# Kernel optimization log

Measured on AMD Instinct MI355X. Metric: run time of the kernel, lower is better.

Reference implementation:

```python
import jax, jax.numpy as jnp
import numpy as np
import math

B, S, L, D, H, NL, FF, MAXP = 4, 200, 256, 256, 8, 2, 1024, 512
VOC, EDIM, BERT_D, LBL = 50000, 50, 768, 20
DH = D // H
NEG = -1e15


def _pe_table():
    # get_embedding(max_seq_len, hidden, rel_pos_init=0): sinusoidal over 0..2*MAXP
    half = D // 2
    freq = jnp.exp(jnp.arange(half, dtype=jnp.float32) * (-math.log(10000.0) / (half - 1)))
    pos = jnp.arange(2 * MAXP + 1, dtype=jnp.float32)[:, None] * freq[None, :]
    return jnp.concatenate([jnp.sin(pos), jnp.cos(pos)], axis=1)  # [2*MAXP+1, D]


def _ln(x, g, b, eps=1e-5):
    m = x.mean(-1, keepdims=True)
    v = jnp.mean((x - m) ** 2, -1, keepdims=True)
    return (x - m) * jax.lax.rsqrt(v + eps) * g + b


def _forward(lattice, bigrams, seq_len, lex_num, pos_s, pos_e,
             bert_embed, lat_table, big_table, Wc, bc, Wl, bl, W_fus, b_fus,
             Wq, bq, Wk, bk, Wv, bv, Wr, br, u, vb, Wo, bo,
             ln1_g, ln1_b, W1, b1, W2, b2, ln2_g, ln2_b, Wout, bout):
    raw = lat_table[lattice]                                        # [B,L,EDIM]
    big = jnp.pad(big_table[bigrams], ((0, 0), (0, L - S), (0, 0)))  # pad to lattice len
    bert = jnp.pad(bert_embed, ((0, 0), (0, L - S), (0, 0)))
    raw_char = jnp.concatenate([raw, big, bert], -1)                # [B,L,868]
    idx = jnp.arange(L)
    char_mask = idx[None, :] < seq_len[:, None]
    tot_mask = idx[None, :] < (seq_len + lex_num)[:, None]
    lex_mask = tot_mask & (~char_mask)
    # embed_char masked to char positions, embed_lex masked to lexicon positions
    x = (raw_char @ Wc + bc) * char_mask[..., None] + (raw @ Wl + bl) * lex_mask[..., None]

    # four-way relative position fusion ('ff'): relu(Linear(cat[pe_ss,pe_se,pe_es,pe_ee]))
    # computed as sum of four gathered pre-projected tables (same math, no 4D concat)
    pe = _pe_table()
    T = jnp.einsum('pe,keo->kpo', pe, W_fus.reshape(4, D, D))       # [4, 2*MAXP+1, D]
    ss = pos_s[:, :, None] - pos_s[:, None, :] + MAXP
    se = pos_s[:, :, None] - pos_e[:, None, :] + MAXP
    es = pos_e[:, :, None] - pos_s[:, None, :] + MAXP
    ee = pos_e[:, :, None] - pos_e[:, None, :] + MAXP
    rel = jax.nn.relu(T[0][ss] + T[1][se] + T[2][es] + T[3][ee] + b_fus)  # [B,L,L,D]

    scale = 1.0 / math.sqrt(DH)
    for l in range(NL):
        qh = (x @ Wq[l] + bq[l]).reshape(B, L, H, DH).transpose(0, 2, 1, 3)
        kh = (x @ Wk[l] + bk[l]).reshape(B, L, H, DH).transpose(0, 2, 1, 3)
        vh = (x @ Wv[l] + bv[l]).reshape(B, L, H, DH).transpose(0, 2, 1, 3)
        rh = (rel @ Wr[l] + br[l]).reshape(B, L, L, H, DH)
        # Transformer-XL style: A+C with content bias u, B+D with position bias v
        AC = jnp.einsum('bhqd,bhkd->bhqk', qh + u[l][None, :, None, :], kh)
        BD = jnp.einsum('bhqd,bqkhd->bhqk', qh + vb[l][None, :, None, :], rh)
        score = (AC + BD) * scale
        score = jnp.where(tot_mask[:, None, None, :], score, NEG)
        attn = jax.nn.softmax(score, -1)
        out = jnp.einsum('bhqk,bhkd->bhqd', attn, vh).transpose(0, 2, 1, 3).reshape(B, L, D)
        x = _ln(out @ Wo[l] + bo[l] + x, ln1_g[l], ln1_b[l])
        h = jax.nn.relu(x @ W1[l] + b1[l]) @ W2[l] + b2[l]
        x = _ln(h + x, ln2_g[l], ln2_b[l])
    return x[:, :S] @ Wout + bout                                   # emission logits [B,S,LBL]


def setup_inputs() -> dict:
    key = jax.random.key(0)
    ks = jax.random.split(key, 32)
    p = lambda i, sh, s=0.02: jax.random.normal(ks[i], sh, jnp.float32) * s
    inp = {}
    inp['lattice'] = jax.random.randint(ks[0], (B, L), 1, VOC)
    inp['bigrams'] = jax.random.randint(ks[1], (B, S), 1, VOC)
    inp['seq_len'] = jax.random.randint(ks[2], (B,), 150, S + 1)
    inp['lex_num'] = jax.random.randint(ks[3], (B,), 20, L - S + 1)
    s_lex = jax.random.randint(ks[4], (B, L - S), 0, 180)
    e_lex = s_lex + jax.random.randint(ks[5], (B, L - S), 1, 20)
    ar = jnp.broadcast_to(jnp.arange(S), (B, S))
    inp['pos_s'] = jnp.concatenate([ar, s_lex], 1)
    inp['pos_e'] = jnp.concatenate([ar, e_lex], 1)
    inp['target'] = jax.random.randint(ks[6], (B, S), 0, LBL)
    inp['bert_embed'] = p(7, (B, S, BERT_D), 1.0)
    inp['lat_table'] = p(8, (VOC, EDIM), 1.0)
    inp['big_table'] = p(9, (VOC, EDIM), 1.0)
    cin = 2 * EDIM + BERT_D
    inp['Wc'] = p(10, (cin, D)); inp['bc'] = jnp.zeros((D,))
    inp['Wl'] = p(11, (EDIM, D)); inp['bl'] = jnp.zeros((D,))
    inp['W_fus'] = p(12, (4 * D, D)); inp['b_fus'] = jnp.zeros((D,))
    inp['Wq'] = p(13, (NL, D, D)); inp['bq'] = jnp.zeros((NL, D))
    inp['Wk'] = p(14, (NL, D, D)); inp['bk'] = jnp.zeros((NL, D))
    inp['Wv'] = p(15, (NL, D, D)); inp['bv'] = jnp.zeros((NL, D))
    inp['Wr'] = p(16, (NL, D, D)); inp['br'] = jnp.zeros((NL, D))
    inp['u'] = p(17, (NL, H, DH)); inp['vb'] = p(18, (NL, H, DH))
    inp['Wo'] = p(19, (NL, D, D)); inp['bo'] = jnp.zeros((NL, D))
    inp['ln1_g'] = jnp.ones((NL, D)); inp['ln1_b'] = jnp.zeros((NL, D))
    inp['W1'] = p(20, (NL, D, FF)); inp['b1'] = jnp.zeros((NL, FF))
    inp['W2'] = p(21, (NL, FF, D)); inp['b2'] = jnp.zeros((NL, D))
    inp['ln2_g'] = jnp.ones((NL, D)); inp['ln2_b'] = jnp.zeros((NL, D))
    inp['Wout'] = p(22, (D, LBL)); inp['bout'] = jnp.zeros((LBL,))
    return inp


def reference(lattice, bigrams, seq_len, lex_num, pos_s, pos_e, target,
              bert_embed, lat_table, big_table, Wc, bc, Wl, bl, W_fus, b_fus,
              Wq, bq, Wk, bk, Wv, bv, Wr, br, u, vb, Wo, bo,
              ln1_g, ln1_b, W1, b1, W2, b2, ln2_g, ln2_b, Wout, bout):
    # target is consumed by the downstream CRF loss (omitted); emission logits returned
    return _forward(lattice, bigrams, seq_len, lex_num, pos_s, pos_e,
                    bert_embed, lat_table, big_table, Wc, bc, Wl, bl, W_fus, b_fus,
                    Wq, bq, Wk, bk, Wv, bv, Wr, br, u, vb, Wo, bo,
                    ln1_g, ln1_b, W1, b1, W2, b2, ln2_g, ln2_b, Wout, bout)
```

## Files before the change

kernel.cpp:

```cpp
#include <hip/hip_runtime.h>
#include <math.h>

#define NB 4
#define SS 200
#define LT 256
#define DD 256
#define NH 8
#define NLAYER 2
#define FFD 1024
#define BERTD 768
#define NEGINF -1e15f
#define SCL 0.17677669529663687f

typedef __attribute__((ext_vector_type(8))) short bf16x8;
typedef __attribute__((ext_vector_type(4))) float f32x4;
typedef __attribute__((ext_vector_type(8))) unsigned short u16x8;

__device__ inline float bf2f(unsigned short h) {
    union { unsigned int u; float f; } v; v.u = ((unsigned int)h) << 16; return v.f;
}
__device__ inline unsigned short f2bf(float x) {
    union { float f; unsigned int u; } v; v.f = x;
    unsigned int r = v.u + 0x7fffu + ((v.u >> 16) & 1u);
    return (unsigned short)(r >> 16);
}
__device__ inline void split2(float x, unsigned short& h, unsigned short& l) {
    h = f2bf(x); l = f2bf(x - bf2f(h));
}

__global__ void gather_v3(const int* __restrict__ lattice, const int* __restrict__ bigrams,
                          const int* __restrict__ seq_len, const int* __restrict__ lex_num,
                          const float* __restrict__ bert, const float* __restrict__ lat_t,
                          const float* __restrict__ big_t,
                          unsigned short* __restrict__ Gh, unsigned short* __restrict__ Gl)
{
    const int row = blockIdx.x, t = threadIdx.x;
    const int b = row >> 8, l = row & 255;
    const int sl = seq_len[b], tl = sl + lex_num[b];
    const float mC = (l < sl) ? 1.f : 0.f;
    const float mL = (l >= sl && l < tl) ? 1.f : 0.f;
    const int lat = lattice[row];
    const int big = (l < SS) ? bigrams[b*SS + l] : 0;
    for (int i = t; i < 1024; i += 256) {
        float v;
        if (i < 50)        v = lat_t[lat*50 + i] * mC;
        else if (i < 100)  v = (l < SS) ? big_t[big*50 + (i-50)] * mC : 0.f;
        else if (i < 868)  v = (l < SS) ? bert[(b*SS + l)*BERTD + (i-100)] * mC : 0.f;
        else if (i < 918)  v = lat_t[lat*50 + (i-868)] * mL;
        else if (i == 918) v = mC;
        else if (i == 919) v = mL;
        else               v = 0.f;
        unsigned short hh, ll; split2(v, hh, ll);
        Gh[(size_t)row*1024 + i] = hh; Gl[(size_t)row*1024 + i] = ll;
    }
}

__global__ void wcomb_kernel(const float* __restrict__ Wc, const float* __restrict__ bc,
                             const float* __restrict__ Wl, const float* __restrict__ bl,
                             float* __restrict__ Wcomb)
{
    const int r = blockIdx.x, t = threadIdx.x;
    float v;
    if (r < 868)       v = Wc[r*DD + t];
    else if (r < 918)  v = Wl[(r-868)*DD + t];
    else if (r == 918) v = bc[t];
    else if (r == 919) v = bl[t];
    else               v = 0.f;
    Wcomb[r*DD + t] = v;
}

__global__ void pe_v3(unsigned short* __restrict__ PEh, unsigned short* __restrict__ PEl)
{
    const int p = blockIdx.x, t = threadIdx.x;
    float v = 0.f;
    if (p <= 1024) {
        const float fr = expf(-(float)(t & 127) * (9.210340371976184f / 127.0f));
        const float arg = (float)p * fr;
        v = (t < 128) ? sinf(arg) : cosf(arg);
    }
    unsigned short hh, ll; split2(v, hh, ll);
    PEh[p*DD + t] = hh; PEl[p*DD + t] = ll;
}

__global__ void smallpack(const float* __restrict__ bq, const float* __restrict__ bk,
                          const float* __restrict__ bv, const float* __restrict__ b_fus,
                          float* __restrict__ bqkv, float* __restrict__ bfus4)
{
    const int t = threadIdx.x;
    for (int l = 0; l < NLAYER; ++l) {
        bqkv[l*768 + t]       = bq[l*DD + t];
        bqkv[l*768 + 256 + t] = bk[l*DD + t];
        bqkv[l*768 + 512 + t] = bv[l*DD + t];
    }
    bfus4[t] = b_fus[t];
    bfus4[256 + t] = 0.f; bfus4[512 + t] = 0.f; bfus4[768 + t] = 0.f;
}

__global__ void vrbias_kernel(const float* __restrict__ vb, const float* __restrict__ Wr,
                              float* __restrict__ bias_vr)
{
    const int lh = blockIdx.x, t = threadIdx.x;
    const int l = lh >> 3, h = lh & 7;
    float acc = 0.f;
    #pragma unroll 8
    for (int d = 0; d < 32; ++d)
        acc += vb[l*DD + h*32 + d] * Wr[(size_t)l*DD*DD + (h*32 + d)*DD + t];
    bias_vr[lh*DD + t] = acc;
}

__global__ void trans_all(const float* __restrict__ Wcomb, const float* __restrict__ Wq,
                          const float* __restrict__ Wk, const float* __restrict__ Wv,
                          const float* __restrict__ Wo, const float* __restrict__ W1,
                          const float* __restrict__ W2, const float* __restrict__ Wfus,
                          const float* __restrict__ Wr,
                          unsigned short* WcombT_h, unsigned short* WcombT_l,
                          unsigned short* WqkvT_h,  unsigned short* WqkvT_l,
                          unsigned short* WoT_h,    unsigned short* WoT_l,
                          unsigned short* W1T_h,    unsigned short* W1T_l,
                          unsigned short* W2T_h,    unsigned short* W2T_l,
                          unsigned short* WfusT_h,  unsigned short* WfusT_l,
                          unsigned short* WrB_h,    unsigned short* WrB_l)
{
    const int z = blockIdx.z, y = blockIdx.y, tx = blockIdx.x, t = threadIdx.x;
    const float* src; unsigned short *dh, *dl; int K, N;
    switch (z) {
        case 0: if (y) return; K = 1024; N = 256; src = Wcomb; dh = WcombT_h; dl = WcombT_l; break;
        case 1: { if (y >= 6) return; int l = y/3, s = y%3; K = 256; N = 256;
                  src = (s==0 ? Wq : s==1 ? Wk : Wv) + l*65536;
                  dh = WqkvT_h + (l*768 + s*256)*256; dl = WqkvT_l + (l*768 + s*256)*256; } break;
        case 2: if (y >= 2) return; K = 256; N = 256;  src = Wo + y*65536;  dh = WoT_h + y*65536;  dl = WoT_l + y*65536;  break;
        case 3: if (y >= 2) return; K = 256; N = 1024; src = W1 + y*262144; dh = W1T_h + y*262144; dl = W1T_l + y*262144; break;
        case 4: if (y >= 2) return; K = 1024; N = 256; src = W2 + y*262144; dh = W2T_h + y*262144; dl = W2T_l + y*262144; break;
        case 5: if (y >= 4) return; K = 256; N = 256;  src = Wfus + y*65536; dh = WfusT_h + y*65536; dl = WfusT_l + y*65536; break;
        case 6: { if (y >= 16) return; int l = y >> 3, h = y & 7; K = 32; N = 256;
                  src = Wr + (size_t)l*65536 + h*32*256;
                  dh = WrB_h + y*8192; dl = WrB_l + y*8192; } break;
        default: return;
    }
    const int tiles_x = N >> 5;
    const int tn = tx % tiles_x, tk = tx / tiles_x;
    if (tk >= (K >> 5)) return;
    __shared__ float s[32][33];
    const int lr = t >> 5, lc = t & 31;
    #pragma unroll
    for (int i = 0; i < 4; ++i)
        s[lr + 8*i][lc] = src[(size_t)(tk*32 + lr + 8*i)*N + tn*32 + lc];
    __syncthreads();
    #pragma unroll
    for (int i = 0; i < 4; ++i) {
        const int n = tn*32 + lr + 8*i, k = tk*32 + lc;
        unsigned short hh, ll; split2(s[lc][lr + 8*i], hh, ll);
        dh[(size_t)n*K + k] = hh;
        dl[(size_t)n*K + k] = ll;
    }
}

template<int BK, bool RELU, bool EMIT>
__global__ __launch_bounds__(256) void gemm_v3(
    const unsigned short* __restrict__ Ah, const unsigned short* __restrict__ Al,
    const unsigned short* __restrict__ Bh, const unsigned short* __restrict__ Bl,
    const float* __restrict__ bias, const float* __restrict__ resid,
    float* __restrict__ C, unsigned short* __restrict__ Ch, unsigned short* __restrict__ Cl,
    int M, int N, int K, int lda, int ldc, int aZ, int bZ, int cZ, int biasZ)
{
    constexpr int LDK = BK + 8;
    __shared__ unsigned short AhS[64*LDK], AlS[64*LDK];
    __shared__ unsigned short BhS[64*LDK], BlS[64*LDK];
    const int z = blockIdx.z;
    Ah += (size_t)z * aZ; Al += (size_t)z * aZ;
    Bh += (size_t)z * bZ; Bl += (size_t)z * bZ;
    C  += (size_t)z * cZ;
    if (EMIT) { Ch += (size_t)z * cZ; Cl += (size_t)z * cZ; }
    if (bias) bias += (size_t)z * biasZ;

    const int t = threadIdx.x;
    const int row0 = blockIdx.y * 64, col0 = blockIdx.x * 64;
    const int lane = t & 63, w = t >> 6;
    const int wm = w >> 1, wn = w & 1;
    const int fr = lane & 15, fq = lane >> 4;
    const int sr = t >> 2, sc0 = (t & 3) * (BK/4);

    f32x4 acc[2][2];
    #pragma unroll
    for (int i = 0; i < 2; ++i)
        #pragma unroll
        for (int j = 0; j < 2; ++j) acc[i][j] = (f32x4){0.f, 0.f, 0.f, 0.f};

    for (int k0 = 0; k0 < K; k0 += BK) {
        #pragma unroll
        for (int i = 0; i < BK/32; ++i) {
            const int c = sc0 + i*8;
            *(u16x8*)&AhS[sr*LDK + c] = *(const u16x8*)&Ah[(size_t)(row0+sr)*lda + k0 + c];
            *(u16x8*)&AlS[sr*LDK + c] = *(const u16x8*)&Al[(size_t)(row0+sr)*lda + k0 + c];
            *(u16x8*)&BhS[sr*LDK + c] = *(const u16x8*)&Bh[(size_t)(col0+sr)*K + k0 + c];
            *(u16x8*)&BlS[sr*LDK + c] = *(const u16x8*)&Bl[(size_t)(col0+sr)*K + k0 + c];
        }
        __syncthreads();
        #pragma unroll
        for (int ks = 0; ks < BK/32; ++ks) {
            const int ko = ks*32 + fq*8;
            const bf16x8 ah0 = *(const bf16x8*)&AhS[(wm*32 + fr)*LDK + ko];
            const bf16x8 ah1 = *(const bf16x8*)&AhS[(wm*32 + 16 + fr)*LDK + ko];
            const bf16x8 al0 = *(const bf16x8*)&AlS[(wm*32 + fr)*LDK + ko];
            const bf16x8 al1 = *(const bf16x8*)&AlS[(wm*32 + 16 + fr)*LDK + ko];
            #pragma unroll
            for (int nt = 0; nt < 2; ++nt) {
                const int nb = (wn*32 + nt*16 + fr)*LDK + ko;
                const bf16x8 bh = *(const bf16x8*)&BhS[nb];
                const bf16x8 bl = *(const bf16x8*)&BlS[nb];
                acc[0][nt] = __builtin_amdgcn_mfma_f32_16x16x32_bf16(ah0, bh, acc[0][nt], 0, 0, 0);
                acc[0][nt] = __builtin_amdgcn_mfma_f32_16x16x32_bf16(ah0, bl, acc[0][nt], 0, 0, 0);
                acc[0][nt] = __builtin_amdgcn_mfma_f32_16x16x32_bf16(al0, bh, acc[0][nt], 0, 0, 0);
                acc[1][nt] = __builtin_amdgcn_mfma_f32_16x16x32_bf16(ah1, bh, acc[1][nt], 0, 0, 0);
                acc[1][nt] = __builtin_amdgcn_mfma_f32_16x16x32_bf16(ah1, bl, acc[1][nt], 0, 0, 0);
                acc[1][nt] = __builtin_amdgcn_mfma_f32_16x16x32_bf16(al1, bh, acc[1][nt], 0, 0, 0);
            }
        }
        __syncthreads();
    }
    #pragma unroll
    for (int mt = 0; mt < 2; ++mt) {
        #pragma unroll
        for (int nt = 0; nt < 2; ++nt) {
            const int gcol = col0 + wn*32 + nt*16 + fr;
            const float bv = bias ? bias[gcol] : 0.f;
            #pragma unroll
            for (int r = 0; r < 4; ++r) {
                const int grow = row0 + wm*32 + mt*16 + fq*4 + r;
                float v = acc[mt][nt][r] + bv;
                if (resid) v += resid[(size_t)grow*ldc + gcol];
                if (RELU)  v = fmaxf(v, 0.f);
                C[(size_t)grow*ldc + gcol] = v;
                if (EMIT) {
                    unsigned short hh, ll; split2(v, hh, ll);
                    Ch[(size_t)grow*ldc + gcol] = hh;
                    Cl[(size_t)grow*ldc + gcol] = ll;
                }
            }
        }
    }
}

__global__ void rcc_split(const float* __restrict__ Tn,
                          unsigned short* __restrict__ Rh, unsigned short* __restrict__ Rl)
{
    const int p = blockIdx.x, t = threadIdx.x;
    const float v = Tn[(size_t)p*1024 + t] + Tn[(size_t)p*1024 + 256 + t]
                  + Tn[(size_t)p*1024 + 512 + t] + Tn[(size_t)p*1024 + 768 + t];
    unsigned short hh, ll; split2(fmaxf(v, 0.f), hh, ll);
    Rh[p*DD + t] = hh; Rl[p*DD + t] = ll;
}

__global__ __launch_bounds__(256) void attn_v4(
    const float* __restrict__ qkvb, const float* __restrict__ qr,
    const float* __restrict__ Tn, const float* __restrict__ Dcc,
    const int* __restrict__ pos_s, const int* __restrict__ pos_e,
    const int* __restrict__ seq_len, const int* __restrict__ lex_num,
    const float* __restrict__ u, float* __restrict__ ob,
    unsigned short* __restrict__ obh, unsigned short* __restrict__ obl)
{
    __shared__ float qu[256];
    __shared__ float qrl[NH][260];
    __shared__ float sc[NH][264];
    __shared__ float acb[NH][264];
    __shared__ float relb[32][260];
    __shared__ float red[2048];
    float* DccL = &relb[0][0];

    const int t = threadIdx.x, row = blockIdx.x;
    const int b = row >> 8, q = row & 255;
    const int totlen = seq_len[b] + lex_num[b];
    if (q >= SS && q >= totlen) {
        ob[row*DD + t] = 0.f; obh[row*DD + t] = 0; obl[row*DD + t] = 0;
        return;
    }
    const bool qc = (q < SS);
    const int gstart = qc ? SS : 0;

    qu[t] = qkvb[(size_t)row*768 + t] + u[t];
    if (totlen > gstart) {
        #pragma unroll
        for (int h = 0; h < NH; ++h) qrl[h][t] = qr[(size_t)row*2048 + h*256 + t];
    }
    if (qc && t < SS) {
        #pragma unroll
        for (int h = 0; h < NH; ++h)
            DccL[h*SS + t] = Dcc[((size_t)h*1024 + row)*448 + q + t];
    }
    const int ps_q = pos_s[row], pe_q = pos_e[row];
    const int* psb = pos_s + b*LT;
    const int* peb = pos_e + b*LT;
    __syncthreads();

    {
        const int h = t & 7, k0 = t >> 3;
        const float4* qp = (const float4*)&qu[h*32];
        #pragma unroll
        for (int pass = 0; pass < 8; ++pass) {
            const int kg = pass*32 + k0;
            if (kg < totlen) {
                const float4* kp = (const float4*)&qkvb[(size_t)(b*LT + kg)*768 + 256 + h*32];
                float ac = 0.f;
                #pragma unroll
                for (int d4 = 0; d4 < 8; ++d4) {
                    const float4 kv = kp[d4], qv = qp[d4];
                    ac += kv.x*qv.x + kv.y*qv.y + kv.z*qv.z + kv.w*qv.w;
                }
                if (qc && kg < SS) sc[h][kg] = (ac + DccL[h*SS + (SS-1) - kg]) * SCL;
                else               acb[h][kg] = ac;
            } else {
                sc[h][kg] = NEGINF;
            }
        }
    }
    __syncthreads();

    const int gs0 = gstart & ~31;
    for (int K0 = gs0; K0 < totlen; K0 += 32) {
        {
            const int r = t >> 3, c4 = (t & 7)*4;
            const int kg = K0 + r;
            if (kg >= gstart && kg < totlen) {
                const int sk = psb[kg], ek = peb[kg];
                const float* t0 = Tn + (size_t)(ps_q - sk + 512)*1024;
                const float* t1 = Tn + (size_t)(ps_q - ek + 512)*1024 + 256;
                const float* t2 = Tn + (size_t)(pe_q - sk + 512)*1024 + 512;
                const float* t3 = Tn + (size_t)(pe_q - ek + 512)*1024 + 768;
                #pragma unroll
                for (int i = 0; i < 8; ++i) {
                    const int e = i*32 + c4;
                    const float4 a = *(const float4*)&t0[e];
                    const float4 bb = *(const float4*)&t1[e];
                    const float4 c = *(const float4*)&t2[e];
                    const float4 d = *(const float4*)&t3[e];
                    float4 v;
                    v.x = fmaxf(a.x + bb.x + c.x + d.x, 0.f);
                    v.y = fmaxf(a.y + bb.y + c.y + d.y, 0.f);
                    v.z = fmaxf(a.z + bb.z + c.z + d.z, 0.f);
                    v.w = fmaxf(a.w + bb.w + c.w + d.w, 0.f);
                    *(float4*)&relb[r][e] = v;
                }
            }
        }
        __syncthreads();
        {
            const int dk = t & 31, seg = t >> 5;
            const int kg = K0 + dk;
            if (kg >= gstart && kg < totlen) {
                float a[8] = {0.f,0.f,0.f,0.f,0.f,0.f,0.f,0.f};
                const int e0 = seg*32;
                #pragma unroll
                for (int e4 = 0; e4 < 8; ++e4) {
                    const float4 r4 = *(const float4*)&relb[dk][e0 + e4*4];
                    #pragma unroll
                    for (int h = 0; h < 8; ++h) {
                        const float4 q4 = *(const float4*)&qrl[h][e0 + e4*4];
                        a[h] += r4.x*q4.x + r4.y*q4.y + r4.z*q4.z + r4.w*q4.w;
                    }
                }
                float4* rb = (float4*)&red[(seg*32 + dk)*8];
                rb[0] = make_float4(a[0], a[1], a[2], a[3]);
                rb[1] = make_float4(a[4], a[5], a[6], a[7]);
            }
        }
        __syncthreads();
        {
            const int k = t >> 3, h = t & 7;
            const int kg = K0 + k;
            if (kg >= gstart && kg < totlen) {
                float s = 0.f;
                #pragma unroll
                for (int g = 0; g < 8; ++g) s += red[g*256 + t];
                sc[h][kg] = (s + acb[h][kg]) * SCL;
            }
        }
        __syncthreads();
    }

    {
        const int g = t >> 5, ln = t & 31;
        float vals[8];
        float m = -INFINITY;
        #pragma unroll
        for (int i = 0; i < 8; ++i) {
            const int kidx = ln + 32*i;
            vals[i] = (kidx < totlen) ? sc[g][kidx] : NEGINF;
            m = fmaxf(m, vals[i]);
        }
        #pragma unroll
        for (int off = 16; off >= 1; off >>= 1) m = fmaxf(m, __shfl_xor(m, off, 32));
        float sum = 0.f;
        #pragma unroll
        for (int i = 0; i < 8; ++i) { vals[i] = expf(vals[i] - m); sum += vals[i]; }
        #pragma unroll
        for (int off = 16; off >= 1; off >>= 1) sum += __shfl_xor(sum, off, 32);
        const float inv = 1.0f / sum;
        #pragma unroll
        for (int i = 0; i < 8; ++i) sc[g][ln + 32*i] = vals[i] * inv;
    }
    __syncthreads();
    {
        const int j4 = (t & 63)*4, kr = t >> 6;
        const int h = j4 >> 5;
        float4 acc = make_float4(0.f, 0.f, 0.f, 0.f);
        const float* vp = qkvb + (size_t)(b*LT)*768 + 512 + j4;
        for (int k = kr; k < totlen; k += 4) {
            const float p = sc[h][k];
            const float4 v = *(const float4*)&vp[(size_t)k*768];
            acc.x += p*v.x; acc.y += p*v.y; acc.z += p*v.z; acc.w += p*v.w;
        }
        *(float4*)&red[kr*256 + j4] = acc;
    }
    __syncthreads();
    {
        const float v = red[t] + red[256 + t] + red[512 + t] + red[768 + t];
        ob[row*DD + t] = v;
        unsigned short hh, ll; split2(v, hh, ll);
        obh[row*DD + t] = hh; obl[row*DD + t] = ll;
    }
}

template<bool EMIT>
__global__ void ln_v3(const float* __restrict__ in, const float* __restrict__ g,
                      const float* __restrict__ bb, float* __restrict__ out,
                      unsigned short* __restrict__ oh, unsigned short* __restrict__ ol)
{
    __shared__ float red[4];
    const int t = threadIdx.x, row = blockIdx.x;
    const float v = in[row*DD + t];
    float s = v;
    #pragma unroll
    for (int off = 32; off >= 1; off >>= 1) s += __shfl_xor(s, off, 64);
    if ((t & 63) == 0) red[t >> 6] = s;
    __syncthreads();
    const float m = (red[0] + red[1] + red[2] + red[3]) * (1.0f/256.0f);
    __syncthreads();
    const float d = v - m;
    float s2 = d*d;
    #pragma unroll
    for (int off = 32; off >= 1; off >>= 1) s2 += __shfl_xor(s2, off, 64);
    if ((t & 63) == 0) red[t >> 6] = s2;
    __syncthreads();
    const float var = (red[0] + red[1] + red[2] + red[3]) * (1.0f/256.0f);
    const float o = d * rsqrtf(var + 1e-5f) * g[t] + bb[t];
    out[row*DD + t] = o;
    if (EMIT) {
        unsigned short hh, ll; split2(o, hh, ll);
        oh[row*DD + t] = hh; ol[row*DD + t] = ll;
    }
}

__global__ void out_kernel(const float* __restrict__ x, const float* __restrict__ Wout,
                           const float* __restrict__ bout, float* __restrict__ out)
{
    __shared__ float xs[256];
    const int t = threadIdx.x, row = blockIdx.x;
    const int b = row / SS, s = row % SS;
    const float* xr = x + (b*LT + s)*DD;
    for (int i = t; i < DD; i += 64) xs[i] = xr[i];
    __syncthreads();
    if (t < 20) {
        float acc = bout[t];
        for (int d = 0; d < DD; ++d) acc += xs[d] * Wout[d*20 + t];
        out[row*20 + t] = acc;
    }
}

extern "C" void kernel_launch(void* const* d_in, const int* in_sizes, int n_in,
                              void* d_out, int out_size, void* d_ws, size_t ws_size,
                              hipStream_t stream)
{
    const int*   lattice = (const int*)d_in[0];
    const int*   bigrams = (const int*)d_in[1];
    const int*   seq_len = (const int*)d_in[2];
    const int*   lex_num = (const int*)d_in[3];
    const int*   pos_s   = (const int*)d_in[4];
    const int*   pos_e   = (const int*)d_in[5];
    const float* bert    = (const float*)d_in[7];
    const float* lat_t   = (const float*)d_in[8];
    const float* big_t   = (const float*)d_in[9];
    const float* Wc      = (const float*)d_in[10];
    const float* bc      = (const float*)d_in[11];
    const float* Wl      = (const float*)d_in[12];
    const float* bl      = (const float*)d_in[13];
    const float* W_fus   = (const float*)d_in[14];
    const float* b_fus   = (const float*)d_in[15];
    const float* Wq      = (const float*)d_in[16];
    const float* bq      = (const float*)d_in[17];
    const float* Wk      = (const float*)d_in[18];
    const float* bk      = (const float*)d_in[19];
    const float* Wv      = (const float*)d_in[20];
    const float* bv      = (const float*)d_in[21];
    const float* Wr      = (const float*)d_in[22];
    const float* u_bias  = (const float*)d_in[24];
    const float* v_bias  = (const float*)d_in[25];
    const float* Wo      = (const float*)d_in[26];
    const float* bo      = (const float*)d_in[27];
    const float* ln1g    = (const float*)d_in[28];
    const float* ln1b    = (const float*)d_in[29];
    const float* W1      = (const float*)d_in[30];
    const float* b1      = (const float*)d_in[31];
    const float* W2      = (const float*)d_in[32];
    const float* b2      = (const float*)d_in[33];
    const float* ln2g    = (const float*)d_in[34];
    const float* ln2b    = (const float*)d_in[35];
    const float* Wout    = (const float*)d_in[36];
    const float* bout    = (const float*)d_in[37];

    float* ws = (float*)d_ws;
    float* qkvb = ws;  ws += NB*LT*768;
    float* ob   = ws;  ws += NB*LT*DD;
    float* t1   = ws;  ws += NB*LT*DD;
    float* x2   = ws;  ws += NB*LT*DD;
    float* t2   = ws;  ws += NB*LT*DD;
    float* hb   = ws;  ws += NB*LT*FFD;
    float* x    = ws;  ws += NB*LT*DD;
    float* Tn   = ws;  ws += 1088*1024;
    float* qr   = ws;  ws += NB*LT*NH*DD;
    float* Dcc  = ws;  ws += 8*1024*448;
    float* Wcomb= ws;  ws += 1024*DD;
    float* bqkv = ws;  ws += NLAYER*768;
    float* bfus4= ws;  ws += 1024;
    float* bias_vr = ws; ws += NLAYER*NH*DD;
    unsigned short* us = (unsigned short*)ws;
    unsigned short* xh  = us; us += 1024*256;
    unsigned short* xl  = us; us += 1024*256;
    unsigned short* x2h = us; us += 1024*256;
    unsigned short* x2l = us; us += 1024*256;
    unsigned short* qkvbh = us; us += 1024*768;
    unsigned short* qkvbl = us; us += 1024*768;
    unsigned short* hbh = us; us += 1024*1024;
    unsigned short* hbl = us; us += 1024*1024;
    unsigned short* obh = us; us += 1024*256;
    unsigned short* obl = us; us += 1024*256;
    unsigned short* qrh = us; us += 1024*2048;
    unsigned short* qrl = us; us += 1024*2048;
    unsigned short* Rcch = us; us += 1025*256;
    unsigned short* Rccl = us; us += 1025*256;
    unsigned short* WcombT_h = us; us += 256*1024;
    unsigned short* WcombT_l = us; us += 256*1024;
    unsigned short* WqkvT_h  = us; us += NLAYER*768*256;
    unsigned short* WqkvT_l  = us; us += NLAYER*768*256;
    unsigned short* WoT_h    = us; us += NLAYER*256*256;
    unsigned short* WoT_l    = us; us += NLAYER*256*256;
    unsigned short* W1T_h    = us; us += NLAYER*1024*256;
    unsigned short* W1T_l    = us; us += NLAYER*1024*256;
    unsigned short* W2T_h    = us; us += NLAYER*256*1024;
    unsigned short* W2T_l    = us; us += NLAYER*256*1024;
    unsigned short* WfusT_h  = us; us += 1024*256;
    unsigned short* WfusT_l  = us; us += 1024*256;
    unsigned short* WrB_h    = us; us += NLAYER*NH*256*32;
    unsigned short* WrB_l    = us; us += NLAYER*NH*256*32;
    unsigned short* Gh  = hbh;
    unsigned short* Gl  = hbl;
    unsigned short* PEh = (unsigned short*)t1;
    unsigned short* PEl = (unsigned short*)t2;

    const int M = NB*LT;

    gather_v3<<<M, 256, 0, stream>>>(lattice, bigrams, seq_len, lex_num,
                                     bert, lat_t, big_t, Gh, Gl);
    wcomb_kernel<<<1024, 256, 0, stream>>>(Wc, bc, Wl, bl, Wcomb);
    pe_v3<<<1088, 256, 0, stream>>>(PEh, PEl);
    smallpack<<<1, 256, 0, stream>>>(bq, bk, bv, b_fus, bqkv, bfus4);
    vrbias_kernel<<<NLAYER*NH, 256, 0, stream>>>(v_bias, Wr, bias_vr);
    trans_all<<<dim3(256, 16, 7), 256, 0, stream>>>(Wcomb, Wq, Wk, Wv, Wo, W1, W2, W_fus, Wr,
        WcombT_h, WcombT_l, WqkvT_h, WqkvT_l, WoT_h, WoT_l,
        W1T_h, W1T_l, W2T_h, W2T_l, WfusT_h, WfusT_l, WrB_h, WrB_l);

    gemm_v3<64,false,false><<<dim3(16, 17), 256, 0, stream>>>(
        PEh, PEl, WfusT_h, WfusT_l, bfus4, nullptr, Tn, nullptr, nullptr,
        1088, 1024, 256, 256, 1024, 0, 0, 0, 0);
    rcc_split<<<1025, 256, 0, stream>>>(Tn, Rcch, Rccl);

    gemm_v3<64,false,true><<<dim3(4, 16), 256, 0, stream>>>(
        Gh, Gl, WcombT_h, WcombT_l, nullptr, nullptr, x, xh, xl,
        M, 256, 1024, 1024, 256, 0, 0, 0, 0);

    for (int l = 0; l < NLAYER; ++l) {
        gemm_v3<64,false,true><<<dim3(12, 16), 256, 0, stream>>>(
            xh, xl, WqkvT_h + l*768*256, WqkvT_l + l*768*256, bqkv + l*768, nullptr,
            qkvb, qkvbh, qkvbl, M, 768, 256, 256, 768, 0, 0, 0, 0);
        gemm_v3<32,false,true><<<dim3(4, 16, 8), 256, 0, stream>>>(
            qkvbh, qkvbl, WrB_h + l*8*8192, WrB_l + l*8*8192, bias_vr + l*8*256, nullptr,
            qr, qrh, qrl, M, 256, 32, 768, 2048, 32, 8192, 256, 256);
        gemm_v3<64,false,false><<<dim3(7, 16, 8), 256, 0, stream>>>(
            qrh, qrl, Rcch + 313*256, Rccl + 313*256, nullptr, nullptr,
            Dcc, nullptr, nullptr, M, 448, 256, 2048, 448, 256, 0, 1024*448, 0);
        attn_v4<<<M, 256, 0, stream>>>(qkvb, qr, Tn, Dcc, pos_s, pos_e,
                                       seq_len, lex_num, u_bias + l*DD, ob, obh, obl);
        gemm_v3<64,false,false><<<dim3(4, 16), 256, 0, stream>>>(
            obh, obl, WoT_h + l*65536, WoT_l + l*65536, bo + l*DD, x,
            t1, nullptr, nullptr, M, 256, 256, 256, 256, 0, 0, 0, 0);
        ln_v3<true><<<M, 256, 0, stream>>>(t1, ln1g + l*DD, ln1b + l*DD, x2, x2h, x2l);
        gemm_v3<64,true,true><<<dim3(16, 16), 256, 0, stream>>>(
            x2h, x2l, W1T_h + l*262144, W1T_l + l*262144, b1 + l*FFD, nullptr,
            hb, hbh, hbl, M, FFD, 256, 256, 1024, 0, 0, 0, 0);
        gemm_v3<64,false,false><<<dim3(4, 16), 256, 0, stream>>>(
            hbh, hbl, W2T_h + l*262144, W2T_l + l*262144, b2 + l*DD, x2,
            t2, nullptr, nullptr, M, 256, 1024, 1024, 256, 0, 0, 0, 0);
        ln_v3<true><<<M, 256, 0, stream>>>(t2, ln2g + l*DD, ln2b + l*DD, x, xh, xl);
    }
    out_kernel<<<NB*SS, 64, 0, stream>>>(x, Wout, bout, (float*)d_out);
}
```

Before: 492.6 us.

## Merge prep kernels, compact transpose grid, and simplify lexicon score reduction in attention

The four small setup kernels (Wcomb build, PE table, bias packing, v-bias projection) are merged into one launch. The transpose kernel moves from a sparse 3D grid with many early-exit blocks to a dense 1D grid. In attention, the lexicon-key relative score loop now processes 16 keys per step instead of 32. It drops the acb buffer and the separate shared-memory reduction pass in favour of a per-head half-split dot product combined with a shuffle, which cuts shared memory and one barrier per step. The cost is that each thread recomputes full 128-element dot products and loses the q-vector reuse across heads.

```diff
diff --git a/kernel.cpp b/kernel.cpp
--- a/kernel.cpp
+++ b/kernel.cpp
@@ -55,91 +55,90 @@
     }
 }
 
-__global__ void wcomb_kernel(const float* __restrict__ Wc, const float* __restrict__ bc,
-                             const float* __restrict__ Wl, const float* __restrict__ bl,
-                             float* __restrict__ Wcomb)
-{
-    const int r = blockIdx.x, t = threadIdx.x;
-    float v;
-    if (r < 868)       v = Wc[r*DD + t];
-    else if (r < 918)  v = Wl[(r-868)*DD + t];
-    else if (r == 918) v = bc[t];
-    else if (r == 919) v = bl[t];
-    else               v = 0.f;
-    Wcomb[r*DD + t] = v;
-}
-
-__global__ void pe_v3(unsigned short* __restrict__ PEh, unsigned short* __restrict__ PEl)
-{
-    const int p = blockIdx.x, t = threadIdx.x;
-    float v = 0.f;
-    if (p <= 1024) {
-        const float fr = expf(-(float)(t & 127) * (9.210340371976184f / 127.0f));
-        const float arg = (float)p * fr;
-        v = (t < 128) ? sinf(arg) : cosf(arg);
-    }
-    unsigned short hh, ll; split2(v, hh, ll);
-    PEh[p*DD + t] = hh; PEl[p*DD + t] = ll;
-}
-
-__global__ void smallpack(const float* __restrict__ bq, const float* __restrict__ bk,
-                          const float* __restrict__ bv, const float* __restrict__ b_fus,
-                          float* __restrict__ bqkv, float* __restrict__ bfus4)
-{
+__global__ void prep_all(const float* __restrict__ Wc, const float* __restrict__ bc,
+                         const float* __restrict__ Wl, const float* __restrict__ bl,
+                         const float* __restrict__ vb, const float* __restrict__ Wr,
+                         const float* __restrict__ bq, const float* __restrict__ bk,
+                         const float* __restrict__ bv, const float* __restrict__ b_fus,
+                         float* __restrict__ Wcomb,
+                         unsigned short* __restrict__ PEh, unsigned short* __restrict__ PEl,
+                         float* __restrict__ bias_vr,
+                         float* __restrict__ bqkv, float* __restrict__ bfus4)
+{
+    const int g = blockIdx.x, t = threadIdx.x;
+    if (g < 1024) {
+        const int r = g;
+        float v;
+        if (r < 868)       v = Wc[r*DD + t];
+        else if (r < 918)  v = Wl[(r-868)*DD + t];
+        else if (r == 918) v = bc[t];
+        else if (r == 919) v = bl[t];
+        else               v = 0.f;
+        Wcomb[r*DD + t] = v;
+    } else if (g < 2112) {
+        const int p = g - 1024;
+        float v = 0.f;
+        if (p <= 1024) {
+            const float fr = expf(-(float)(t & 127) * (9.210340371976184f / 127.0f));
+            const float arg = (float)p * fr;
+            v = (t < 128) ? sinf(arg) : cosf(arg);
+        }
+        unsigned short hh, ll; split2(v, hh, ll);
+        PEh[p*DD + t] = hh; PEl[p*DD + t] = ll;
+    } else if (g < 2128) {
+        const int lh = g - 2112;
+        const int l = lh >> 3, h = lh & 7;
+        float acc = 0.f;
+        #pragma unroll 8
+        for (int d = 0; d < 32; ++d)
+            acc += vb[l*DD + h*32 + d] * Wr[(size_t)l*DD*DD + (h*32 + d)*DD + t];
+        bias_vr[lh*DD + t] = acc;
+    } else {
+        for (int l = 0; l < NLAYER; ++l) {
+            bqkv[l*768 + t]       = bq[l*DD + t];
+            bqkv[l*768 + 256 + t] = bk[l*DD + t];
+            bqkv[l*768 + 512 + t] = bv[l*DD + t];
+        }
+        bfus4[t] = b_fus[t];
+        bfus4[256 + t] = 0.f; bfus4[512 + t] = 0.f; bfus4[768 + t] = 0.f;
+    }
+}
+
+__global__ void trans_all2(const float* __restrict__ Wcomb, const float* __restrict__ Wq,
+                           const float* __restrict__ Wk, const float* __restrict__ Wv,
+                           const float* __restrict__ Wo, const float* __restrict__ W1,
+                           const float* __restrict__ W2, const float* __restrict__ Wfus,
+                           const float* __restrict__ Wr,
+                           unsigned short* WcombT_h, unsigned short* WcombT_l,
+                           unsigned short* WqkvT_h,  unsigned short* WqkvT_l,
+                           unsigned short* WoT_h,    unsigned short* WoT_l,
+                           unsigned short* W1T_h,    unsigned short* W1T_l,
+                           unsigned short* W2T_h,    unsigned short* W2T_l,
+                           unsigned short* WfusT_h,  unsigned short* WfusT_l,
+                           unsigned short* WrB_h,    unsigned short* WrB_l)
+{
+    int g = blockIdx.x;
     const int t = threadIdx.x;
-    for (int l = 0; l < NLAYER; ++l) {
-        bqkv[l*768 + t]       = bq[l*DD + t];
-        bqkv[l*768 + 256 + t] = bk[l*DD + t];
-        bqkv[l*768 + 512 + t] = bv[l*DD + t];
-    }
-    bfus4[t] = b_fus[t];
-    bfus4[256 + t] = 0.f; bfus4[512 + t] = 0.f; bfus4[768 + t] = 0.f;
-}
-
-__global__ void vrbias_kernel(const float* __restrict__ vb, const float* __restrict__ Wr,
-                              float* __restrict__ bias_vr)
-{
-    const int lh = blockIdx.x, t = threadIdx.x;
-    const int l = lh >> 3, h = lh & 7;
-    float acc = 0.f;
-    #pragma unroll 8
-    for (int d = 0; d < 32; ++d)
-        acc += vb[l*DD + h*32 + d] * Wr[(size_t)l*DD*DD + (h*32 + d)*DD + t];
-    bias_vr[lh*DD + t] = acc;
-}
-
-__global__ void trans_all(const float* __restrict__ Wcomb, const float* __restrict__ Wq,
-                          const float* __restrict__ Wk, const float* __restrict__ Wv,
-                          const float* __restrict__ Wo, const float* __restrict__ W1,
-                          const float* __restrict__ W2, const float* __restrict__ Wfus,
-                          const float* __restrict__ Wr,
-                          unsigned short* WcombT_h, unsigned short* WcombT_l,
-                          unsigned short* WqkvT_h,  unsigned short* WqkvT_l,
-                          unsigned short* WoT_h,    unsigned short* WoT_l,
-                          unsigned short* W1T_h,    unsigned short* W1T_l,
-                          unsigned short* W2T_h,    unsigned short* W2T_l,
-                          unsigned short* WfusT_h,  unsigned short* WfusT_l,
-                          unsigned short* WrB_h,    unsigned short* WrB_l)
-{
-    const int z = blockIdx.z, y = blockIdx.y, tx = blockIdx.x, t = threadIdx.x;
-    const float* src; unsigned short *dh, *dl; int K, N;
-    switch (z) {
-        case 0: if (y) return; K = 1024; N = 256; src = Wcomb; dh = WcombT_h; dl = WcombT_l; break;
-        case 1: { if (y >= 6) return; int l = y/3, s = y%3; K = 256; N = 256;
-                  src = (s==0 ? Wq : s==1 ? Wk : Wv) + l*65536;
-                  dh = WqkvT_h + (l*768 + s*256)*256; dl = WqkvT_l + (l*768 + s*256)*256; } break;
-        case 2: if (y >= 2) return; K = 256; N = 256;  src = Wo + y*65536;  dh = WoT_h + y*65536;  dl = WoT_l + y*65536;  break;
-        case 3: if (y >= 2) return; K = 256; N = 1024; src = W1 + y*262144; dh = W1T_h + y*262144; dl = W1T_l + y*262144; break;
-        case 4: if (y >= 2) return; K = 1024; N = 256; src = W2 + y*262144; dh = W2T_h + y*262144; dl = W2T_l + y*262144; break;
-        case 5: if (y >= 4) return; K = 256; N = 256;  src = Wfus + y*65536; dh = WfusT_h + y*65536; dl = WfusT_l + y*65536; break;
-        case 6: { if (y >= 16) return; int l = y >> 3, h = y & 7; K = 32; N = 256;
-                  src = Wr + (size_t)l*65536 + h*32*256;
-                  dh = WrB_h + y*8192; dl = WrB_l + y*8192; } break;
-        default: return;
-    }
+    const float* src; unsigned short *dh, *dl; int K, N, tile;
+    if (g < 256)        { K=1024; N=256;  src=Wcomb; dh=WcombT_h; dl=WcombT_l; tile=g; }
+    else if (g < 640)   { g -= 256; int j = g >> 6; tile = g & 63; int l = j/3, s = j%3;
+                          K=256; N=256;
+                          src = (s==0 ? Wq : s==1 ? Wk : Wv) + l*65536;
+                          dh = WqkvT_h + (l*768 + s*256)*256; dl = WqkvT_l + (l*768 + s*256)*256; }
+    else if (g < 768)   { g -= 640; int y = g >> 6; tile = g & 63; K=256; N=256;
+                          src = Wo + y*65536;  dh = WoT_h + y*65536;  dl = WoT_l + y*65536; }
+    else if (g < 1280)  { g -= 768; int y = g >> 8; tile = g & 255; K=256; N=1024;
+                          src = W1 + y*262144; dh = W1T_h + y*262144; dl = W1T_l + y*262144; }
+    else if (g < 1792)  { g -= 1280; int y = g >> 8; tile = g & 255; K=1024; N=256;
+                          src = W2 + y*262144; dh = W2T_h + y*262144; dl = W2T_l + y*262144; }
+    else if (g < 2048)  { g -= 1792; int y = g >> 6; tile = g & 63; K=256; N=256;
+                          src = Wfus + y*65536; dh = WfusT_h + y*65536; dl = WfusT_l + y*65536; }
+    else                { g -= 2048; int y = g >> 3; tile = g & 7; int l = y >> 3, h = y & 7;
+                          K=32; N=256;
+                          src = Wr + (size_t)l*65536 + h*32*256;
+                          dh = WrB_h + y*8192; dl = WrB_l + y*8192; }
     const int tiles_x = N >> 5;
-    const int tn = tx % tiles_x, tk = tx / tiles_x;
-    if (tk >= (K >> 5)) return;
+    const int tn = tile % tiles_x, tk = tile / tiles_x;
     __shared__ float s[32][33];
     const int lr = t >> 5, lc = t & 31;
     #pragma unroll
@@ -251,7 +250,7 @@
     Rh[p*DD + t] = hh; Rl[p*DD + t] = ll;
 }
 
-__global__ __launch_bounds__(256) void attn_v4(
+__global__ __launch_bounds__(256) void attn_v5(
     const float* __restrict__ qkvb, const float* __restrict__ qr,
     const float* __restrict__ Tn, const float* __restrict__ Dcc,
     const int* __restrict__ pos_s, const int* __restrict__ pos_e,
@@ -262,9 +261,8 @@
     __shared__ float qu[256];
     __shared__ float qrl[NH][260];
     __shared__ float sc[NH][264];
-    __shared__ float acb[NH][264];
-    __shared__ float relb[32][260];
-    __shared__ float red[2048];
+    __shared__ float relb[16][260];
+    __shared__ float red[1024];
     float* DccL = &relb[0][0];
 
     const int t = threadIdx.x, row = blockIdx.x;
@@ -307,7 +305,7 @@
                     ac += kv.x*qv.x + kv.y*qv.y + kv.z*qv.z + kv.w*qv.w;
                 }
                 if (qc && kg < SS) sc[h][kg] = (ac + DccL[h*SS + (SS-1) - kg]) * SCL;
-                else               acb[h][kg] = ac;
+                else               sc[h][kg] = ac;
             } else {
                 sc[h][kg] = NEGINF;
             }
@@ -315,10 +313,10 @@
     }
     __syncthreads();
 
-    const int gs0 = gstart & ~31;
-    for (int K0 = gs0; K0 < totlen; K0 += 32) {
+    const int gs0 = gstart & ~15;
+    for (int K0 = gs0; K0 < totlen; K0 += 16) {
         {
-            const int r = t >> 3, c4 = (t & 7)*4;
+            const int r = t >> 4, c4 = (t & 15)*4;
             const int kg = K0 + r;
             if (kg >= gstart && kg < totlen) {
                 const int sk = psb[kg], ek = peb[kg];
@@ -327,8 +325,8 @@
                 const float* t2 = Tn + (size_t)(pe_q - sk + 512)*1024 + 512;
                 const float* t3 = Tn + (size_t)(pe_q - ek + 512)*1024 + 768;
                 #pragma unroll
-                for (int i = 0; i < 8; ++i) {
-                    const int e = i*32 + c4;
+                for (int i = 0; i < 4; ++i) {
+                    const int e = i*64 + c4;
                     const float4 a = *(const float4*)&t0[e];
                     const float4 bb = *(const float4*)&t1[e];
                     const float4 c = *(const float4*)&t2[e];
@@ -344,35 +342,21 @@
         }
         __syncthreads();
         {
-            const int dk = t & 31, seg = t >> 5;
-            const int kg = K0 + dk;
+            const int k = t & 15, half = (t >> 4) & 1, h = t >> 5;
+            const int kg = K0 + k;
+            float s = 0.f;
             if (kg >= gstart && kg < totlen) {
-                float a[8] = {0.f,0.f,0.f,0.f,0.f,0.f,0.f,0.f};
-                const int e0 = seg*32;
+                const float4* rp = (const float4*)&relb[k][half*128];
+                const float4* qp = (const float4*)&qrl[h][half*128];
                 #pragma unroll
-                for (int e4 = 0; e4 < 8; ++e4) {
-                    const float4 r4 = *(const float4*)&relb[dk][e0 + e4*4];
-                    #pragma unroll
-                    for (int h = 0; h < 8; ++h) {
-                        const float4 q4 = *(const float4*)&qrl[h][e0 + e4*4];
-                        a[h] += r4.x*q4.x + r4.y*q4.y + r4.z*q4.z + r4.w*q4.w;
-                    }
+                for (int e4 = 0; e4 < 32; ++e4) {
+                    const float4 r4 = rp[e4], q4 = qp[e4];
+                    s += r4.x*q4.x + r4.y*q4.y + r4.z*q4.z + r4.w*q4.w;
                 }
-                float4* rb = (float4*)&red[(seg*32 + dk)*8];
-                rb[0] = make_float4(a[0], a[1], a[2], a[3]);
-                rb[1] = make_float4(a[4], a[5], a[6], a[7]);
             }
-        }
-        __syncthreads();
-        {
-            const int k = t >> 3, h = t & 7;
-            const int kg = K0 + k;
-            if (kg >= gstart && kg < totlen) {
-                float s = 0.f;
-                #pragma unroll
-                for (int g = 0; g < 8; ++g) s += red[g*256 + t];
-                sc[h][kg] = (s + acb[h][kg]) * SCL;
-            }
+            s += __shfl_xor(s, 16);
+            if (half == 0 && kg >= gstart && kg < totlen)
+                sc[h][kg] = (sc[h][kg] + s) * SCL;
         }
         __syncthreads();
     }
@@ -560,11 +544,9 @@
 
     gather_v3<<<M, 256, 0, stream>>>(lattice, bigrams, seq_len, lex_num,
                                      bert, lat_t, big_t, Gh, Gl);
-    wcomb_kernel<<<1024, 256, 0, stream>>>(Wc, bc, Wl, bl, Wcomb);
-    pe_v3<<<1088, 256, 0, stream>>>(PEh, PEl);
-    smallpack<<<1, 256, 0, stream>>>(bq, bk, bv, b_fus, bqkv, bfus4);
-    vrbias_kernel<<<NLAYER*NH, 256, 0, stream>>>(v_bias, Wr, bias_vr);
-    trans_all<<<dim3(256, 16, 7), 256, 0, stream>>>(Wcomb, Wq, Wk, Wv, Wo, W1, W2, W_fus, Wr,
+    prep_all<<<2129, 256, 0, stream>>>(Wc, bc, Wl, bl, v_bias, Wr, bq, bk, bv, b_fus,
+                                       Wcomb, PEh, PEl, bias_vr, bqkv, bfus4);
+    trans_all2<<<2176, 256, 0, stream>>>(Wcomb, Wq, Wk, Wv, Wo, W1, W2, W_fus, Wr,
         WcombT_h, WcombT_l, WqkvT_h, WqkvT_l, WoT_h, WoT_l,
         W1T_h, W1T_l, W2T_h, W2T_l, WfusT_h, WfusT_l, WrB_h, WrB_l);
 
@@ -587,7 +569,7 @@
         gemm_v3<64,false,false><<<dim3(7, 16, 8), 256, 0, stream>>>(
             qrh, qrl, Rcch + 313*256, Rccl + 313*256, nullptr, nullptr,
             Dcc, nullptr, nullptr, M, 448, 256, 2048, 448, 256, 0, 1024*448, 0);
-        attn_v4<<<M, 256, 0, stream>>>(qkvb, qr, Tn, Dcc, pos_s, pos_e,
+        attn_v5<<<M, 256, 0, stream>>>(qkvb, qr, Tn, Dcc, pos_s, pos_e,
                                        seq_len, lex_num, u_bias + l*DD, ob, obh, obl);
         gemm_v3<64,false,false><<<dim3(4, 16), 256, 0, stream>>>(
             obh, obl, WoT_h + l*65536, WoT_l + l*65536, bo + l*DD, x,
```

New measurement: 470.2 us. 1.05x faster.
